# Kernel optimization log

Measured on AMD Instinct MI355X. Metric: run time of the kernel, lower is better.

Reference implementation:

```python
import jax, jax.numpy as jnp
import numpy as np

N, T, SAMPLES, OUT = 128, 1024, 1024, 8
TWO_PI = 2.0 * np.pi


def setup_inputs() -> dict:
    key = jax.random.key(0)
    ks = jax.random.split(key, 7)
    inp = jax.random.normal(ks[0], (N, T, 3), dtype=jnp.float32)
    h1, h2 = SAMPLES // 2, SAMPLES // 8
    W1 = jax.random.normal(ks[1], (h1, SAMPLES), dtype=jnp.float32) / np.sqrt(SAMPLES)
    b1 = jax.random.normal(ks[2], (h1,), dtype=jnp.float32) * 0.01
    W2 = jax.random.normal(ks[3], (h2, h1), dtype=jnp.float32) / np.sqrt(h1)
    b2 = jax.random.normal(ks[4], (h2,), dtype=jnp.float32) * 0.01
    W3 = jax.random.normal(ks[5], (OUT, h2), dtype=jnp.float32) / np.sqrt(h2)
    b3 = jax.random.normal(ks[6], (OUT,), dtype=jnp.float32) * 0.01
    return {"inp": inp, "W1": W1, "b1": b1, "W2": W2, "b2": b2, "W3": W3, "b3": b3}


def reference(inp, W1, b1, W2, b2, W3, b3):
    samples = W1.shape[1]
    t_len = inp.shape[1]
    x = inp[:, :, 0]          # [N, T] real signal
    day = inp[:, :, 2]        # [N, T] non-uniform times
    freqs = jnp.linspace(0.0, float(t_len - 1), samples, dtype=jnp.float32)
    # phase[n, s, t] = -2*pi * f_s * day[n, t]
    phase = (-TWO_PI) * freqs[None, :, None] * day[:, None, :]
    # complex exp split into real/imag panes; bmm fourier @ x -> [N, S]
    re = jnp.einsum('nst,nt->ns', jnp.cos(phase), x)
    im = jnp.einsum('nst,nt->ns', jnp.sin(phase), x)
    frequential = jnp.sqrt(re * re + im * im)  # |F x|, [N, samples]
    # 3-layer MLP with sigmoid activations (dropout = identity in eval)
    h = jax.nn.sigmoid(frequential @ W1.T + b1)
    h = jax.nn.sigmoid(h @ W2.T + b2)
    return h @ W3.T + b3
```

## Files before the change

### kernel.cpp

```cpp
#include <hip/hip_runtime.h>
#include <math.h>

#define NN   128
#define TT   1024
#define SS   1024
#define H1D  512
#define H2D  128
#define OUTD 8
#define KQN  8

#define MR    2048
#define WHALF 5
#define ALPHA 0.3702402f
#define BETA  6.35556e-6f
#define DSCALE 0.3432943f

#define OFF_SUBT 0
#define OFF_P1   (NN*512*4*2)

__device__ __forceinline__ float cos_rev(float r) { return __builtin_amdgcn_cosf(r); }
__device__ __forceinline__ float sin_rev(float r) { return __builtin_amdgcn_sinf(r); }

__device__ __forceinline__ float wave_sum(float v) {
#pragma unroll
    for (int off = 32; off > 0; off >>= 1) v += __shfl_xor(v, off, 64);
    return v;
}

__global__ __launch_bounds__(256) void k_sf(const float* __restrict__ inp,
                                            float* __restrict__ ws) {
    const int r   = blockIdx.x;
    const int n   = blockIdx.y;
    const int tid = threadIdx.x;

    __shared__ float2 Ag[512];
    __shared__ float2 Bg[512];

    Ag[tid] = make_float2(0.f, 0.f);
    Ag[tid + 256] = make_float2(0.f, 0.f);
    __syncthreads();

    const float* row = inp + (size_t)n * TT * 3;
#pragma unroll
    for (int pp = 0; pp < 4; ++pp) {
        const int t = pp * 256 + tid;
        const float x  = row[t * 3 + 0];
        const float d  = row[t * 3 + 2];
        const float df = d - floorf(d);
        const float p512 = 512.0f * df;
        const float r512 = p512 - floorf(p512);
        const float cre = x * cos_rev(r512);
        const float cim = -x * sin_rev(r512);
        const float z  = df * 2048.0f;
        const int   j0 = (int)z;
        const float dl = z - (float)j0;
        const int k0 = (r + 5 - j0 + 2048) & 3;
#pragma unroll
        for (int i = 0; i < 3; ++i) {
            const int   k = k0 + 4 * i;
            const float u = dl - (float)(k - WHALF);
            const float w = __expf(-ALPHA * u * u);
            const int  gi = (j0 + k - WHALF) & (MR - 1);
            const int   q = gi >> 2;
            atomicAdd(&Ag[q].x, w * cre);
            atomicAdd(&Ag[q].y, w * cim);
        }
    }
    __syncthreads();

    float2* src = Ag;
    float2* dst = Bg;
#pragma unroll
    for (int s = 0; s < 9; ++s) {
        const int   m    = 1 << s;
        const float invl = 1.0f / (float)(512 >> s);
        const int tau = tid;
        const int j   = tau >> s;
        const float rr = (float)j * invl;
        const float cv = cos_rev(rr), sv = sin_rev(rr);
        const float2 a = src[tau];
        const float2 b = src[tau + 256];
        const int o = tau + (tau & ~(m - 1));
        dst[o] = make_float2(a.x + b.x, a.y + b.y);
        const float dr = a.x - b.x, di = a.y - b.y;
        dst[o + m] = make_float2(fmaf(di, sv, dr * cv),
                                 fmaf(di, cv, -dr * sv));
        __syncthreads();
        float2* tmp = src; src = dst; dst = tmp;
    }

    float2* SUBT = (float2*)(ws + OFF_SUBT);
    SUBT[((size_t)n * 512 + tid)       * 4 + r] = src[tid];
    SUBT[((size_t)n * 512 + tid + 256) * 4 + r] = src[tid + 256];
}

__global__ __launch_bounds__(256) void k_cl1p(const float* __restrict__ W1,
                                              float* __restrict__ ws) {
    const int kq = blockIdx.x;
    const int jq = blockIdx.y;
    const int nb = blockIdx.z;
    const int tid = threadIdx.x;

    __shared__ float4 Al[8][32];
    float* Alf = (float*)Al;
    const float2* SUBT = (const float2*)(ws + OFF_SUBT);
#pragma unroll
    for (int i = 0; i < 4; ++i) {
        const int e    = i * 256 + tid;
        const int rown = e >> 7;
        const int kk   = e & 127;
        const int n    = nb * 8 + rown;
        const int ss   = kq * 128 + kk;
        const int k    = (ss + 1536) & (MR - 1);
        const int km   = ss & 511;
        const float2* F = SUBT + ((size_t)n * 512 + km) * 4;
        float2 X = F[0];
        const float f1 = (float)k * (1.0f / 2048.0f);
#pragma unroll
        for (int rr = 1; rr < 4; ++rr) {
            const float2 Fr = F[rr];
            const float fr = (float)rr * f1;
            const float ff = fr - floorf(fr);
            const float cv = cos_rev(ff), sv = sin_rev(ff);
            X.x = fmaf(Fr.x, cv, fmaf(Fr.y, sv, X.x));
            X.y = fmaf(Fr.y, cv, fmaf(-Fr.x, sv, X.y));
        }
        const int sp = ss - 512;
        const float D = DSCALE * __expf(BETA * (float)(sp * sp));
        Alf[e] = sqrtf(fmaf(X.x, X.x, X.y * X.y)) * D;
    }
    __syncthreads();

    const int jl = tid & 127, ng = tid >> 7;
    const int j = jq * 128 + jl;
    const float4* W1v = (const float4*)W1;
    float a0 = 0.f, a1 = 0.f, a2 = 0.f, a3 = 0.f;
#pragma unroll 4
    for (int k4 = 0; k4 < 32; ++k4) {
        const float4 w  = W1v[(size_t)j * 256 + kq * 32 + k4];
        const float4 x0 = Al[ng * 4 + 0][k4];
        const float4 x1 = Al[ng * 4 + 1][k4];
        const float4 x2 = Al[ng * 4 + 2][k4];
        const float4 x3 = Al[ng * 4 + 3][k4];
        a0 = fmaf(x0.x, w.x, fmaf(x0.y, w.y, fmaf(x0.z, w.z, fmaf(x0.w, w.w, a0))));
        a1 = fmaf(x1.x, w.x, fmaf(x1.y, w.y, fmaf(x1.z, w.z, fmaf(x1.w, w.w, a1))));
        a2 = fmaf(x2.x, w.x, fmaf(x2.y, w.y, fmaf(x2.z, w.z, fmaf(x2.w, w.w, a2))));
        a3 = fmaf(x3.x, w.x, fmaf(x3.y, w.y, fmaf(x3.z, w.z, fmaf(x3.w, w.w, a3))));
    }
    float* P1 = ws + OFF_P1;
    const float acc[4] = {a0, a1, a2, a3};
#pragma unroll
    for (int i = 0; i < 4; ++i)
        P1[((size_t)(kq * NN + nb * 8 + ng * 4 + i)) * H1D + j] = acc[i];
}

__global__ __launch_bounds__(1024) void k_mlp(const float* __restrict__ b1,
                                              const float* __restrict__ W2,
                                              const float* __restrict__ b2,
                                              const float* __restrict__ W3,
                                              const float* __restrict__ b3,
                                              const float* __restrict__ ws,
                                              float* __restrict__ out) {
    const int n   = blockIdx.x;
    const int tid = threadIdx.x;
    const int wid = tid >> 6, lane = tid & 63;

    __shared__ float h1L[H1D];
    __shared__ float h2L[H2D];

    if (tid < H1D) {
        const int j = tid;
        float s = b1[j];
#pragma unroll
        for (int kq = 0; kq < KQN; ++kq)
            s += ws[OFF_P1 + ((size_t)kq * NN + n) * H1D + j];
        h1L[j] = 1.0f / (1.0f + __expf(-s));
    }
    __syncthreads();

    {
        const float4* H1v = (const float4*)h1L;
        const float4 ha = H1v[lane], hb = H1v[64 + lane];
#pragma unroll
        for (int q = 0; q < 8; ++q) {
            const int j = wid * 8 + q;
            const float4* W2v = (const float4*)W2 + (size_t)j * 128;
            const float4 wa = W2v[lane], wb = W2v[64 + lane];
            float a = fmaf(wa.x, ha.x, fmaf(wa.y, ha.y, fmaf(wa.z, ha.z, wa.w * ha.w)));
            a = fmaf(wb.x, hb.x, fmaf(wb.y, hb.y, fmaf(wb.z, hb.z, fmaf(wb.w, hb.w, a))));
            a = wave_sum(a);
            if (lane == 0) h2L[j] = 1.0f / (1.0f + __expf(-(a + b2[j])));
        }
    }
    __syncthreads();

    if (wid < OUTD) {
        const float2 w = ((const float2*)W3)[wid * 64 + lane];
        const float2 h = ((const float2*)h2L)[lane];
        float a = fmaf(w.x, h.x, w.y * h.y);
        a = wave_sum(a);
        if (lane == 0) out[n * OUTD + wid] = a + b3[wid];
    }
}

extern "C" void kernel_launch(void* const* d_in, const int* in_sizes, int n_in,
                              void* d_out, int out_size, void* d_ws, size_t ws_size,
                              hipStream_t stream) {
    (void)in_sizes; (void)n_in; (void)out_size; (void)ws_size;
    const float* inp = (const float*)d_in[0];
    const float* W1  = (const float*)d_in[1];
    const float* b1  = (const float*)d_in[2];
    const float* W2  = (const float*)d_in[3];
    const float* b2  = (const float*)d_in[4];
    const float* W3  = (const float*)d_in[5];
    const float* b3  = (const float*)d_in[6];
    float* out = (float*)d_out;
    float* ws  = (float*)d_ws;

    k_sf  <<<dim3(4, NN),    dim3(256),  0, stream>>>(inp, ws);
    k_cl1p<<<dim3(8, 4, 16), dim3(256),  0, stream>>>(W1, ws);
    k_mlp <<<dim3(NN),       dim3(1024), 0, stream>>>(b1, W2, b2, W3, b3, ws, out);
}
```

Baseline: 43.04 us.

## Fuse MLP tail into layer-1 kernel via last-block atomic counter

```diff
diff --git a/kernel.cpp b/kernel.cpp
--- a/kernel.cpp
+++ b/kernel.cpp
@@ -17,6 +17,7 @@
 
 #define OFF_SUBT 0
 #define OFF_P1   (NN*512*4*2)
+#define OFF_CNT  (OFF_P1 + KQN*NN*H1D)
 
 __device__ __forceinline__ float cos_rev(float r) { return __builtin_amdgcn_cosf(r); }
 __device__ __forceinline__ float sin_rev(float r) { return __builtin_amdgcn_sinf(r); }
@@ -32,6 +33,8 @@
     const int r   = blockIdx.x;
     const int n   = blockIdx.y;
     const int tid = threadIdx.x;
+
+    if (r == 0 && n < 16 && tid == 0) ((int*)(ws + OFF_CNT))[n] = 0;
 
     __shared__ float2 Ag[512];
     __shared__ float2 Bg[512];
@@ -95,13 +98,24 @@
 }
 
 __global__ __launch_bounds__(256) void k_cl1p(const float* __restrict__ W1,
-                                              float* __restrict__ ws) {
+                                              const float* __restrict__ b1,
+                                              const float* __restrict__ W2,
+                                              const float* __restrict__ b2,
+                                              const float* __restrict__ W3,
+                                              const float* __restrict__ b3,
+                                              float* __restrict__ ws,
+                                              float* __restrict__ out) {
     const int kq = blockIdx.x;
     const int jq = blockIdx.y;
     const int nb = blockIdx.z;
     const int tid = threadIdx.x;
+    const int wid = tid >> 6, lane = tid & 63;
 
     __shared__ float4 Al[8][32];
+    __shared__ float  h1L[8][H1D];
+    __shared__ float  h2L[8][H2D];
+    __shared__ int    lastFlag;
+
     float* Alf = (float*)Al;
     const float2* SUBT = (const float2*)(ws + OFF_SUBT);
 #pragma unroll
@@ -131,75 +145,87 @@
     }
     __syncthreads();
 
-    const int jl = tid & 127, ng = tid >> 7;
-    const int j = jq * 128 + jl;
-    const float4* W1v = (const float4*)W1;
-    float a0 = 0.f, a1 = 0.f, a2 = 0.f, a3 = 0.f;
+    {
+        const int jl = tid & 127, ng = tid >> 7;
+        const int j = jq * 128 + jl;
+        const float4* W1v = (const float4*)W1;
+        float a0 = 0.f, a1 = 0.f, a2 = 0.f, a3 = 0.f;
 #pragma unroll 4
-    for (int k4 = 0; k4 < 32; ++k4) {
-        const float4 w  = W1v[(size_t)j * 256 + kq * 32 + k4];
-        const float4 x0 = Al[ng * 4 + 0][k4];
-        const float4 x1 = Al[ng * 4 + 1][k4];
-        const float4 x2 = Al[ng * 4 + 2][k4];
-        const float4 x3 = Al[ng * 4 + 3][k4];
-        a0 = fmaf(x0.x, w.x, fmaf(x0.y, w.y, fmaf(x0.z, w.z, fmaf(x0.w, w.w, a0))));
-        a1 = fmaf(x1.x, w.x, fmaf(x1.y, w.y, fmaf(x1.z, w.z, fmaf(x1.w, w.w, a1))));
-        a2 = fmaf(x2.x, w.x, fmaf(x2.y, w.y, fmaf(x2.z, w.z, fmaf(x2.w, w.w, a2))));
-        a3 = fmaf(x3.x, w.x, fmaf(x3.y, w.y, fmaf(x3.z, w.z, fmaf(x3.w, w.w, a3))));
-    }
-    float* P1 = ws + OFF_P1;
-    const float acc[4] = {a0, a1, a2, a3};
-#pragma unroll
-    for (int i = 0; i < 4; ++i)
-        P1[((size_t)(kq * NN + nb * 8 + ng * 4 + i)) * H1D + j] = acc[i];
-}
-
-__global__ __launch_bounds__(1024) void k_mlp(const float* __restrict__ b1,
-                                              const float* __restrict__ W2,
-                                              const float* __restrict__ b2,
-                                              const float* __restrict__ W3,
-                                              const float* __restrict__ b3,
-                                              const float* __restrict__ ws,
-                                              float* __restrict__ out) {
-    const int n   = blockIdx.x;
-    const int tid = threadIdx.x;
-    const int wid = tid >> 6, lane = tid & 63;
-
-    __shared__ float h1L[H1D];
-    __shared__ float h2L[H2D];
-
-    if (tid < H1D) {
-        const int j = tid;
-        float s = b1[j];
-#pragma unroll
-        for (int kq = 0; kq < KQN; ++kq)
-            s += ws[OFF_P1 + ((size_t)kq * NN + n) * H1D + j];
-        h1L[j] = 1.0f / (1.0f + __expf(-s));
-    }
-    __syncthreads();
-
-    {
-        const float4* H1v = (const float4*)h1L;
-        const float4 ha = H1v[lane], hb = H1v[64 + lane];
-#pragma unroll
-        for (int q = 0; q < 8; ++q) {
-            const int j = wid * 8 + q;
+        for (int k4 = 0; k4 < 32; ++k4) {
+            const float4 w  = W1v[(size_t)j * 256 + kq * 32 + k4];
+            const float4 x0 = Al[ng * 4 + 0][k4];
+            const float4 x1 = Al[ng * 4 + 1][k4];
+            const float4 x2 = Al[ng * 4 + 2][k4];
+            const float4 x3 = Al[ng * 4 + 3][k4];
+            a0 = fmaf(x0.x, w.x, fmaf(x0.y, w.y, fmaf(x0.z, w.z, fmaf(x0.w, w.w, a0))));
+            a1 = fmaf(x1.x, w.x, fmaf(x1.y, w.y, fmaf(x1.z, w.z, fmaf(x1.w, w.w, a1))));
+            a2 = fmaf(x2.x, w.x, fmaf(x2.y, w.y, fmaf(x2.z, w.z, fmaf(x2.w, w.w, a2))));
+            a3 = fmaf(x3.x, w.x, fmaf(x3.y, w.y, fmaf(x3.z, w.z, fmaf(x3.w, w.w, a3))));
+        }
+        float* P1 = ws + OFF_P1;
+        const float acc[4] = {a0, a1, a2, a3};
+#pragma unroll
+        for (int i = 0; i < 4; ++i)
+            P1[((size_t)(kq * NN + nb * 8 + ng * 4 + i)) * H1D + jq * 128 + (tid & 127)] = acc[i];
+    }
+
+    __threadfence();
+    __syncthreads();
+    if (tid == 0) {
+        const int old = atomicAdd(&((int*)(ws + OFF_CNT))[nb], 1);
+        lastFlag = (old == 31);
+    }
+    __syncthreads();
+    if (!lastFlag) return;
+    __threadfence();
+
+    {
+        const float* P1 = ws + OFF_P1;
+#pragma unroll
+        for (int i = 0; i < 16; ++i) {
+            const int idx = i * 256 + tid;
+            const int ln = idx >> 9, j = idx & 511;
+            const int n = nb * 8 + ln;
+            float s = b1[j];
+#pragma unroll
+            for (int q = 0; q < KQN; ++q)
+                s += P1[((size_t)(q * NN + n)) * H1D + j];
+            h1L[ln][j] = 1.0f / (1.0f + __expf(-s));
+        }
+    }
+    __syncthreads();
+
+    {
+#pragma unroll 2
+        for (int j8 = 0; j8 < 32; ++j8) {
+            const int j = wid * 32 + j8;
             const float4* W2v = (const float4*)W2 + (size_t)j * 128;
             const float4 wa = W2v[lane], wb = W2v[64 + lane];
-            float a = fmaf(wa.x, ha.x, fmaf(wa.y, ha.y, fmaf(wa.z, ha.z, wa.w * ha.w)));
-            a = fmaf(wb.x, hb.x, fmaf(wb.y, hb.y, fmaf(wb.z, hb.z, fmaf(wb.w, hb.w, a))));
+            const float bj = b2[j];
+#pragma unroll
+            for (int ln = 0; ln < 8; ++ln) {
+                const float4* H1v = (const float4*)(&h1L[ln][0]);
+                const float4 ha = H1v[lane], hb = H1v[64 + lane];
+                float a = fmaf(wa.x, ha.x, fmaf(wa.y, ha.y, fmaf(wa.z, ha.z, wa.w * ha.w)));
+                a = fmaf(wb.x, hb.x, fmaf(wb.y, hb.y, fmaf(wb.z, hb.z, fmaf(wb.w, hb.w, a))));
+                a = wave_sum(a);
+                if (lane == 0) h2L[ln][j] = 1.0f / (1.0f + __expf(-(a + bj)));
+            }
+        }
+    }
+    __syncthreads();
+
+    {
+#pragma unroll
+        for (int i = 0; i < 16; ++i) {
+            const int task = wid * 16 + i;
+            const int ln = task >> 3, o = task & 7;
+            const float2 w = ((const float2*)W3)[o * 64 + lane];
+            const float2 h = ((const float2*)(&h2L[ln][0]))[lane];
+            float a = fmaf(w.x, h.x, w.y * h.y);
             a = wave_sum(a);
-            if (lane == 0) h2L[j] = 1.0f / (1.0f + __expf(-(a + b2[j])));
-        }
-    }
-    __syncthreads();
-
-    if (wid < OUTD) {
-        const float2 w = ((const float2*)W3)[wid * 64 + lane];
-        const float2 h = ((const float2*)h2L)[lane];
-        float a = fmaf(w.x, h.x, w.y * h.y);
-        a = wave_sum(a);
-        if (lane == 0) out[n * OUTD + wid] = a + b3[wid];
+            if (lane == 0) out[(nb * 8 + ln) * OUTD + o] = a + b3[o];
+        }
     }
 }
 
@@ -217,7 +243,6 @@
     float* out = (float*)d_out;
     float* ws  = (float*)d_ws;
 
-    k_sf  <<<dim3(4, NN),    dim3(256),  0, stream>>>(inp, ws);
-    k_cl1p<<<dim3(8, 4, 16), dim3(256),  0, stream>>>(W1, ws);
-    k_mlp <<<dim3(NN),       dim3(1024), 0, stream>>>(b1, W2, b2, W3, b3, ws, out);
-}
+    k_sf  <<<dim3(4, NN),    dim3(256), 0, stream>>>(inp, ws);
+    k_cl1p<<<dim3(8, 4, 16), dim3(256), 0, stream>>>(W1, b1, W2, b2, W3, b3, ws, out);
+}
```

Measured after the change: 163.7 us. 3.8x slower.
